# Performance work log

Measured on AMD Instinct MI355X. Metric: run time of the kernel, lower is better.

## Reference

```python
import jax, jax.numpy as jnp
import numpy as np

T, B, D = 2048, 16, 1024  # time, batch, hidden (input_size == output_size)
EPS = 1e-5


def setup_inputs() -> dict:
    key = jax.random.key(0)
    k1, k2 = jax.random.split(key, 2)
    inp = jax.random.normal(k1, (T, B, D), dtype=jnp.float32)
    # nn.Linear(D, 3D, bias=False); stored here as [in, out] so pre = x @ W
    W = jax.random.normal(k2, (D, 3 * D), dtype=jnp.float32) * (1.0 / np.sqrt(D))
    gamma = jnp.ones((3 * D,), dtype=jnp.float32)
    beta = jnp.zeros((3 * D,), dtype=jnp.float32)
    return {"input": inp, "W": W, "gamma": gamma, "beta": beta}


def _linrec(a, b, reverse=False):
    # h_t = a_t * h_{t-1} + b_t  (h_{-1} = 0), parallel prefix over time axis 0
    def comb(c1, c2):
        a1, b1 = c1
        a2, b2 = c2
        return a1 * a2, a2 * b1 + b2
    return jax.lax.associative_scan(comb, (a, b), axis=0, reverse=reverse)[1]


def reference(input, W, gamma, beta):
    d = input.shape[-1]
    pre = jnp.einsum('tbi,io->tbo', input, W)
    # LayerNorm over last dim (3*D)
    mu = pre.mean(-1, keepdims=True)
    var = pre.var(-1, keepdims=True)
    pre = (pre - mu) * jax.lax.rsqrt(var + EPS) * gamma + beta

    g = jax.nn.sigmoid(pre[..., :d])
    x = pre[..., d:2 * d]
    h_gate = jax.nn.sigmoid(pre[..., 2 * d:])

    half = d // 2
    gf, gb = g[..., :half], g[..., half:]
    xf, xb = x[..., :half], x[..., half:]

    h_f = _linrec(1.0 - gf, gf * xf)                 # forward-in-time scan
    h_b = _linrec(1.0 - gb, gb * xb, reverse=True)   # backward-in-time scan
    h = jnp.concatenate([h_f, h_b], axis=-1)         # [T,B,D]
    return (1.0 - h_gate) * h + input * h_gate
```

## Files before the change

### kernel.cpp

```cpp
#include <hip/hip_runtime.h>
#include <hip/hip_bf16.h>
#include <cstdint>

#define T_DIM 2048
#define B_DIM 16
#define D_DIM 1024
#define N3    (3*D_DIM)
#define M_ROWS (T_DIM*B_DIM)
#define HALF  (D_DIM/2)
#define SEG    64
#define SEGLEN (T_DIM/SEG)
#define NSEQ  (2*B_DIM*HALF)
#define NBLK  (N3/256)
#define GEMM_GRID ((M_ROWS/256)*NBLK)

typedef __attribute__((ext_vector_type(8))) short bf16x8;
typedef __attribute__((ext_vector_type(4))) float f32x4;

#define GLD_LDS16(g, l) __builtin_amdgcn_global_load_lds( \
    (const __attribute__((address_space(1))) void*)(g),   \
    (__attribute__((address_space(3))) void*)(l), 16, 0, 0)

__device__ __forceinline__ ushort f2bf(float x) {
    __hip_bfloat16 h = __float2bfloat16(x);
    return *reinterpret_cast<ushort*>(&h);
}

__device__ __forceinline__ float sigmoidf(float x) {
    return 1.0f / (1.0f + __expf(-x));
}

__device__ __forceinline__ float4 ln4(float4 v, float mu, float rs, float4 ga, float4 be) {
    float4 r;
    r.x = (v.x - mu) * rs * ga.x + be.x;
    r.y = (v.y - mu) * rs * ga.y + be.y;
    r.z = (v.z - mu) * rs * ga.z + be.z;
    r.w = (v.w - mu) * rs * ga.w + be.w;
    return r;
}

__device__ __forceinline__ float4 sig4(float4 v) {
    float4 r;
    r.x = sigmoidf(v.x); r.y = sigmoidf(v.y);
    r.z = sigmoidf(v.z); r.w = sigmoidf(v.w);
    return r;
}

__global__ __launch_bounds__(256) void cast_a(const float* __restrict__ in,
                                              ushort* __restrict__ out) {
    const size_t i = (size_t)blockIdx.x * 256 + threadIdx.x;
    const float4* p = (const float4*)in + i * 2;
    float4 a = p[0], b = p[1];
    float f[8] = {a.x, a.y, a.z, a.w, b.x, b.y, b.z, b.w};
    ushort r[8];
#pragma unroll
    for (int j = 0; j < 8; ++j) r[j] = f2bf(f[j]);
    *(uint4*)(out + i * 8) = *(const uint4*)r;
}

__global__ __launch_bounds__(256) void transpose_cast(const float* __restrict__ W,
                                                      ushort* __restrict__ WT) {
    __shared__ float tile[64][65];
    const int c0 = blockIdx.x * 64;
    const int r0 = blockIdx.y * 64;
    const int tr = threadIdx.x >> 6;
    const int tc = threadIdx.x & 63;
#pragma unroll
    for (int i = 0; i < 16; ++i) {
        const int r = tr + i * 4;
        tile[r][tc] = W[(size_t)(r0 + r) * N3 + c0 + tc];
    }
    __syncthreads();
#pragma unroll
    for (int i = 0; i < 16; ++i) {
        const int r = tr + i * 4;
        WT[(size_t)(c0 + r) * D_DIM + r0 + tc] = f2bf(tile[tc][r]);
    }
}

__global__ __launch_bounds__(512, 2) void gemm_bf16(const ushort* __restrict__ A,
                                                    const ushort* __restrict__ BT,
                                                    float* __restrict__ C,
                                                    float2* __restrict__ partial) {
    const int K = D_DIM;
    const int N = N3;
    __shared__ ushort As[2][256 * 64];
    __shared__ ushort Bs[2][256 * 64];
    const int tid  = threadIdx.x;
    const int wave = tid >> 6;
    const int lane = tid & 63;

    int bid = blockIdx.x;
    bid = (bid & 7) * (GEMM_GRID / 8) + (bid >> 3);
    const int m0    = (bid / NBLK) * 256;
    const int n_blk = bid % NBLK;
    const int n0    = n_blk * 256;

    const int wm = wave >> 2;
    const int wn = wave & 3;
    const int srow = lane >> 3;
    const int skc  = (((lane & 7) ^ srow) * 8);

    f32x4 acc[8][4] = {};
    bf16x8 af[8], bfr[4];

    const int q  = lane >> 4;
    const int lm = lane & 15;
    const int sw = lm & 7;

    auto stage = [&](int t, int p) {
#pragma unroll
        for (int it = 0; it < 4; ++it) {
            const int rb = it * 64 + wave * 8;
            GLD_LDS16(A  + (size_t)(m0 + rb + srow) * K + t * 64 + skc, &As[p][rb * 64]);
            GLD_LDS16(BT + (size_t)(n0 + rb + srow) * K + t * 64 + skc, &Bs[p][rb * 64]);
        }
    };
    auto read_frags = [&](int p, int ks) {
        const int ch = ((ks * 4 + q) ^ sw) * 8;
#pragma unroll
        for (int m = 0; m < 8; ++m)
            af[m] = *(const bf16x8*)&As[p][(wm * 128 + m * 16 + lm) * 64 + ch];
#pragma unroll
        for (int n = 0; n < 4; ++n)
            bfr[n] = *(const bf16x8*)&Bs[p][(wn * 64 + n * 16 + lm) * 64 + ch];
    };
    auto do_mfma = [&]() {
        __builtin_amdgcn_s_setprio(1);
#pragma unroll
        for (int m = 0; m < 8; ++m)
#pragma unroll
            for (int n = 0; n < 4; ++n)
                acc[m][n] = __builtin_amdgcn_mfma_f32_16x16x32_bf16(af[m], bfr[n], acc[m][n], 0, 0, 0);
        __builtin_amdgcn_s_setprio(0);
    };

    stage(0, 0);
    stage(1, 1);
    asm volatile("s_waitcnt vmcnt(8)" ::: "memory");
    __builtin_amdgcn_sched_barrier(0);
    __builtin_amdgcn_s_barrier();
    __builtin_amdgcn_sched_barrier(0);

#pragma unroll 2
    for (int t = 0; t < (K / 64) - 2; ++t) {
        const int p = t & 1;
        read_frags(p, 0);
        do_mfma();
        read_frags(p, 1);
        asm volatile("s_waitcnt lgkmcnt(0)" ::: "memory");
        __builtin_amdgcn_sched_barrier(0);
        __builtin_amdgcn_s_barrier();
        __builtin_amdgcn_sched_barrier(0);
        stage(t + 2, p);
        do_mfma();
        asm volatile("s_waitcnt vmcnt(8)" ::: "memory");
        __builtin_amdgcn_sched_barrier(0);
        __builtin_amdgcn_s_barrier();
        __builtin_amdgcn_sched_barrier(0);
    }
    read_frags(0, 0);
    do_mfma();
    read_frags(0, 1);
    do_mfma();
    asm volatile("s_waitcnt vmcnt(0)" ::: "memory");
    __builtin_amdgcn_sched_barrier(0);
    __builtin_amdgcn_s_barrier();
    __builtin_amdgcn_sched_barrier(0);
    read_frags(1, 0);
    do_mfma();
    read_frags(1, 1);
    do_mfma();

#pragma unroll
    for (int m = 0; m < 8; ++m) {
        const int row = m0 + wm * 128 + m * 16 + q * 4;
#pragma unroll
        for (int n = 0; n < 4; ++n) {
            const int col = n0 + wn * 64 + n * 16 + lm;
            float* cp = C + (size_t)row * N + col;
#pragma unroll
            for (int r = 0; r < 4; ++r)
                cp[(size_t)r * N] = acc[m][n][r];
        }
    }

    float* sS  = (float*)&As[0][0];
    float* sSS = sS + 1024;
#pragma unroll
    for (int m = 0; m < 8; ++m) {
#pragma unroll
        for (int r = 0; r < 4; ++r) {
            float s  = acc[m][0][r] + acc[m][1][r] + acc[m][2][r] + acc[m][3][r];
            float ss = acc[m][0][r] * acc[m][0][r] + acc[m][1][r] * acc[m][1][r]
                     + acc[m][2][r] * acc[m][2][r] + acc[m][3][r] * acc[m][3][r];
            s  += __shfl_xor(s, 1);  ss += __shfl_xor(ss, 1);
            s  += __shfl_xor(s, 2);  ss += __shfl_xor(ss, 2);
            s  += __shfl_xor(s, 4);  ss += __shfl_xor(ss, 4);
            s  += __shfl_xor(s, 8);  ss += __shfl_xor(ss, 8);
            if (lm == 0) {
                const int rl = wm * 128 + m * 16 + q * 4 + r;
                sS [wn * 256 + rl] = s;
                sSS[wn * 256 + rl] = ss;
            }
        }
    }
    __syncthreads();
    if (tid < 256) {
        const float S  = sS [tid] + sS [256 + tid] + sS [512 + tid] + sS [768 + tid];
        const float SS = sSS[tid] + sSS[256 + tid] + sSS[512 + tid] + sSS[768 + tid];
        partial[(size_t)n_blk * M_ROWS + m0 + tid] = make_float2(S, SS);
    }
}

__global__ __launch_bounds__(256) void finalize_stats(const float2* __restrict__ partial,
                                                      float2* __restrict__ stats) {
    const int row = blockIdx.x * 256 + threadIdx.x;
    float S = 0.f, SS = 0.f;
#pragma unroll
    for (int nb = 0; nb < NBLK; ++nb) {
        const float2 p = partial[(size_t)nb * M_ROWS + row];
        S += p.x; SS += p.y;
    }
    const float mu  = S * (1.0f / 3072.0f);
    const float var = SS * (1.0f / 3072.0f) - mu * mu;
    stats[row] = make_float2(mu, rsqrtf(var + 1e-5f));
}

__global__ __launch_bounds__(256) void scan_seg(const float* __restrict__ buf,
                                                const float2* __restrict__ stats,
                                                const float* __restrict__ gamma,
                                                const float* __restrict__ beta,
                                                float* __restrict__ segA,
                                                float* __restrict__ segB) {
    const int tid = threadIdx.x;
    const int s   = blockIdx.x;
    const int b   = blockIdx.y;
    const int dir = tid >> 7;
    const int cg4 = tid * 4;
    const float4 ga0 = *(const float4*)&gamma[cg4];
    const float4 be0 = *(const float4*)&beta [cg4];
    const float4 ga1 = *(const float4*)&gamma[cg4 + 1024];
    const float4 be1 = *(const float4*)&beta [cg4 + 1024];
    const size_t base = (size_t)b * N3 + cg4;
    float4 Aa = {1.f, 1.f, 1.f, 1.f};
    float4 Bb = {0.f, 0.f, 0.f, 0.f};

#define SEG_STEP(t)                                                         \
    {   const float2 st = stats[(t) * B_DIM + b];                           \
        const size_t idx = (size_t)(t) * (B_DIM * N3) + base;               \
        const float4 p0 = *(const float4*)&buf[idx];                        \
        const float4 p1 = *(const float4*)&buf[idx + 1024];                 \
        const float4 g  = sig4(ln4(p0, st.x, st.y, ga0, be0));              \
        const float4 xv = ln4(p1, st.x, st.y, ga1, be1);                    \
        Aa.x *= (1.f - g.x); Bb.x = (1.f - g.x) * Bb.x + g.x * xv.x;        \
        Aa.y *= (1.f - g.y); Bb.y = (1.f - g.y) * Bb.y + g.y * xv.y;        \
        Aa.z *= (1.f - g.z); Bb.z = (1.f - g.z) * Bb.z + g.z * xv.z;        \
        Aa.w *= (1.f - g.w); Bb.w = (1.f - g.w) * Bb.w + g.w * xv.w;        }

    if (dir == 0) {
#pragma unroll 4
        for (int i = 0; i < SEGLEN; ++i) SEG_STEP(s * SEGLEN + i);
    } else {
#pragma unroll 4
        for (int i = SEGLEN - 1; i >= 0; --i) SEG_STEP(s * SEGLEN + i);
    }
#undef SEG_STEP
    const int seq = (dir * 16 + b) * HALF + (cg4 - dir * 512);
    *(float4*)&segA[(size_t)s * NSEQ + seq] = Aa;
    *(float4*)&segB[(size_t)s * NSEQ + seq] = Bb;
}

__global__ __launch_bounds__(256) void scan_carry(const float* __restrict__ segA,
                                                  float* __restrict__ segB) {
    const int seq4 = (blockIdx.x * 256 + threadIdx.x) * 4;
    const int dir  = seq4 >> 13;
    float4 h = {0.f, 0.f, 0.f, 0.f};
#define CARRY_STEP(s)                                                       \
    {   const float4 Av = *(const float4*)&segA[(size_t)(s) * NSEQ + seq4]; \
        float4* bp = (float4*)&segB[(size_t)(s) * NSEQ + seq4];             \
        const float4 Bv = *bp;                                              \
        *bp = h;                                                            \
        h.x = Av.x * h.x + Bv.x; h.y = Av.y * h.y + Bv.y;                   \
        h.z = Av.z * h.z + Bv.z; h.w = Av.w * h.w + Bv.w;                   }
    if (dir == 0) {
        for (int s = 0; s < SEG; ++s) CARRY_STEP(s);
    } else {
        for (int s = SEG - 1; s >= 0; --s) CARRY_STEP(s);
    }
#undef CARRY_STEP
}

__global__ __launch_bounds__(256) void scan_apply(const float* __restrict__ buf,
                                                  const float2* __restrict__ stats,
                                                  const float* __restrict__ gamma,
                                                  const float* __restrict__ beta,
                                                  const float* __restrict__ segB,
                                                  const float* __restrict__ input,
                                                  float* __restrict__ out) {
    const int tid = threadIdx.x;
    const int s   = blockIdx.x;
    const int b   = blockIdx.y;
    const int dir = tid >> 7;
    const int cg4 = tid * 4;
    const float4 ga0 = *(const float4*)&gamma[cg4];
    const float4 be0 = *(const float4*)&beta [cg4];
    const float4 ga1 = *(const float4*)&gamma[cg4 + 1024];
    const float4 be1 = *(const float4*)&beta [cg4 + 1024];
    const float4 ga2 = *(const float4*)&gamma[cg4 + 2048];
    const float4 be2 = *(const float4*)&beta [cg4 + 2048];
    const int seq = (dir * 16 + b) * HALF + (cg4 - dir * 512);
    float4 h = *(const float4*)&segB[(size_t)s * NSEQ + seq];
    const size_t base3 = (size_t)b * N3 + cg4;
    const size_t base1 = (size_t)b * D_DIM + cg4;

#define APPLY_STEP(t)                                                       \
    {   const float2 st = stats[(t) * B_DIM + b];                           \
        const size_t i3 = (size_t)(t) * (B_DIM * N3) + base3;               \
        const size_t i1 = (size_t)(t) * (B_DIM * D_DIM) + base1;            \
        const float4 p0 = *(const float4*)&buf[i3];                         \
        const float4 p1 = *(const float4*)&buf[i3 + 1024];                  \
        const float4 p2 = *(const float4*)&buf[i3 + 2048];                  \
        const float4 iv = *(const float4*)&input[i1];                       \
        const float4 g  = sig4(ln4(p0, st.x, st.y, ga0, be0));              \
        const float4 xv = ln4(p1, st.x, st.y, ga1, be1);                    \
        const float4 hg = sig4(ln4(p2, st.x, st.y, ga2, be2));              \
        float4 o;                                                           \
        h.x = (1.f - g.x) * h.x + g.x * xv.x;                               \
        h.y = (1.f - g.y) * h.y + g.y * xv.y;                               \
        h.z = (1.f - g.z) * h.z + g.z * xv.z;                               \
        h.w = (1.f - g.w) * h.w + g.w * xv.w;                               \
        o.x = (1.f - hg.x) * h.x + iv.x * hg.x;                             \
        o.y = (1.f - hg.y) * h.y + iv.y * hg.y;                             \
        o.z = (1.f - hg.z) * h.z + iv.z * hg.z;                             \
        o.w = (1.f - hg.w) * h.w + iv.w * hg.w;                             \
        *(float4*)&out[i1] = o;                                             }

    if (dir == 0) {
#pragma unroll 4
        for (int i = 0; i < SEGLEN; ++i) APPLY_STEP(s * SEGLEN + i);
    } else {
#pragma unroll 4
        for (int i = SEGLEN - 1; i >= 0; --i) APPLY_STEP(s * SEGLEN + i);
    }
#undef APPLY_STEP
}

extern "C" void kernel_launch(void* const* d_in, const int* in_sizes, int n_in,
                              void* d_out, int out_size, void* d_ws, size_t ws_size,
                              hipStream_t stream) {
    const float* input = (const float*)d_in[0];
    const float* W     = (const float*)d_in[1];
    const float* gamma = (const float*)d_in[2];
    const float* beta  = (const float*)d_in[3];
    float* out = (float*)d_out;

    char* ws = (char*)d_ws;
    const size_t szA   = (size_t)M_ROWS * D_DIM * 2;
    const size_t szWT  = (size_t)N3 * D_DIM * 2;
    const size_t szBuf = (size_t)M_ROWS * N3 * 4;
    ushort* Abf  = (ushort*)ws;
    ushort* WT   = (ushort*)(ws + szA);
    float*  buf  = (float*)(ws + szA + szWT);
    float2* partial = (float2*)(ws + szA + szWT + szBuf);
    float2* stats   = (float2*)((char*)partial + (size_t)NBLK * M_ROWS * 8);
    float*  segA = (float*)ws;
    float*  segB = segA + (size_t)SEG * NSEQ;

    cast_a<<<(M_ROWS * D_DIM) / (256 * 8), 256, 0, stream>>>(input, Abf);
    transpose_cast<<<dim3(N3 / 64, D_DIM / 64), 256, 0, stream>>>(W, WT);
    gemm_bf16<<<GEMM_GRID, 512, 0, stream>>>(Abf, WT, buf, partial);
    finalize_stats<<<M_ROWS / 256, 256, 0, stream>>>(partial, stats);
    scan_seg<<<dim3(SEG, B_DIM), 256, 0, stream>>>(buf, stats, gamma, beta, segA, segB);
    scan_carry<<<NSEQ / 1024, 256, 0, stream>>>(segA, segB);
    scan_apply<<<dim3(SEG, B_DIM), 256, 0, stream>>>(buf, stats, gamma, beta, segB, input, out);
}
```

Baseline: 702.1 us.

## Load B fragments directly from pre-packed global layout, retune scan segments

W is repacked into MFMA fragment order so the GEMM loads B fragments straight from global memory into registers instead of staging them through LDS. A now uses a four-deep LDS ring. The scan is split into twice as many segments with deeper unrolling, and the carry pass runs one sequence per thread. Nontemporal loads and stores are used for the large intermediate and output buffers. Register B loads lose LDS sharing across waves and raise global traffic and register pressure.

```diff
diff --git a/kernel.cpp b/kernel.cpp
--- a/kernel.cpp
+++ b/kernel.cpp
@@ -8,7 +8,7 @@
 #define N3    (3*D_DIM)
 #define M_ROWS (T_DIM*B_DIM)
 #define HALF  (D_DIM/2)
-#define SEG    64
+#define SEG    128
 #define SEGLEN (T_DIM/SEG)
 #define NSEQ  (2*B_DIM*HALF)
 #define NBLK  (N3/256)
@@ -30,8 +30,8 @@
     return 1.0f / (1.0f + __expf(-x));
 }
 
-__device__ __forceinline__ float4 ln4(float4 v, float mu, float rs, float4 ga, float4 be) {
-    float4 r;
+__device__ __forceinline__ f32x4 ln4(f32x4 v, float mu, float rs, f32x4 ga, f32x4 be) {
+    f32x4 r;
     r.x = (v.x - mu) * rs * ga.x + be.x;
     r.y = (v.y - mu) * rs * ga.y + be.y;
     r.z = (v.z - mu) * rs * ga.z + be.z;
@@ -39,8 +39,8 @@
     return r;
 }
 
-__device__ __forceinline__ float4 sig4(float4 v) {
-    float4 r;
+__device__ __forceinline__ f32x4 sig4(f32x4 v) {
+    f32x4 r;
     r.x = sigmoidf(v.x); r.y = sigmoidf(v.y);
     r.z = sigmoidf(v.z); r.w = sigmoidf(v.w);
     return r;
@@ -49,8 +49,8 @@
 __global__ __launch_bounds__(256) void cast_a(const float* __restrict__ in,
                                               ushort* __restrict__ out) {
     const size_t i = (size_t)blockIdx.x * 256 + threadIdx.x;
-    const float4* p = (const float4*)in + i * 2;
-    float4 a = p[0], b = p[1];
+    const f32x4* p = (const f32x4*)in + i * 2;
+    f32x4 a = p[0], b = p[1];
     float f[8] = {a.x, a.y, a.z, a.w, b.x, b.y, b.z, b.w};
     ushort r[8];
 #pragma unroll
@@ -58,34 +58,29 @@
     *(uint4*)(out + i * 8) = *(const uint4*)r;
 }
 
-__global__ __launch_bounds__(256) void transpose_cast(const float* __restrict__ W,
-                                                      ushort* __restrict__ WT) {
-    __shared__ float tile[64][65];
-    const int c0 = blockIdx.x * 64;
-    const int r0 = blockIdx.y * 64;
-    const int tr = threadIdx.x >> 6;
-    const int tc = threadIdx.x & 63;
-#pragma unroll
-    for (int i = 0; i < 16; ++i) {
-        const int r = tr + i * 4;
-        tile[r][tc] = W[(size_t)(r0 + r) * N3 + c0 + tc];
-    }
-    __syncthreads();
-#pragma unroll
-    for (int i = 0; i < 16; ++i) {
-        const int r = tr + i * 4;
-        WT[(size_t)(c0 + r) * D_DIM + r0 + tc] = f2bf(tile[tc][r]);
-    }
+__global__ __launch_bounds__(256) void pack_b(const float* __restrict__ W,
+                                              ushort* __restrict__ PB) {
+    const int idx  = blockIdx.x * 256 + threadIdx.x;
+    const int lane = idx & 63;
+    const int gks  = idx >> 6;
+    const int ks   = gks & 31;
+    const int g    = gks >> 5;
+    const int lm = lane & 15, q = lane >> 4;
+    const int n  = g * 16 + lm;
+    const int k0 = ks * 32 + q * 8;
+    ushort r[8];
+#pragma unroll
+    for (int e = 0; e < 8; ++e) r[e] = f2bf(W[(size_t)(k0 + e) * N3 + n]);
+    *(uint4*)&PB[(size_t)idx * 8] = *(const uint4*)r;
 }
 
 __global__ __launch_bounds__(512, 2) void gemm_bf16(const ushort* __restrict__ A,
-                                                    const ushort* __restrict__ BT,
+                                                    const ushort* __restrict__ PB,
                                                     float* __restrict__ C,
                                                     float2* __restrict__ partial) {
     const int K = D_DIM;
     const int N = N3;
-    __shared__ ushort As[2][256 * 64];
-    __shared__ ushort Bs[2][256 * 64];
+    __shared__ ushort As[4][256 * 64];
     const int tid  = threadIdx.x;
     const int wave = tid >> 6;
     const int lane = tid & 63;
@@ -101,76 +96,76 @@
     const int srow = lane >> 3;
     const int skc  = (((lane & 7) ^ srow) * 8);
 
-    f32x4 acc[8][4] = {};
-    bf16x8 af[8], bfr[4];
-
     const int q  = lane >> 4;
     const int lm = lane & 15;
     const int sw = lm & 7;
-
-    auto stage = [&](int t, int p) {
+    const int ch0 = ((0 * 4 + q) ^ sw) * 8;
+    const int ch1 = ((1 * 4 + q) ^ sw) * 8;
+    const int gb  = (n0 >> 4) + wn * 4;
+
+    f32x4 acc[8][4] = {};
+    bf16x8 bA[8], bB[8];
+
+    auto stageA = [&](int t) {
+        const int ts = t > 15 ? 15 : t;
+        const int p  = t & 3;
 #pragma unroll
         for (int it = 0; it < 4; ++it) {
             const int rb = it * 64 + wave * 8;
-            GLD_LDS16(A  + (size_t)(m0 + rb + srow) * K + t * 64 + skc, &As[p][rb * 64]);
-            GLD_LDS16(BT + (size_t)(n0 + rb + srow) * K + t * 64 + skc, &Bs[p][rb * 64]);
+            GLD_LDS16(A + (size_t)(m0 + rb + srow) * K + ts * 64 + skc, &As[p][rb * 64]);
         }
     };
-    auto read_frags = [&](int p, int ks) {
-        const int ch = ((ks * 4 + q) ^ sw) * 8;
-#pragma unroll
-        for (int m = 0; m < 8; ++m)
-            af[m] = *(const bf16x8*)&As[p][(wm * 128 + m * 16 + lm) * 64 + ch];
+    auto loadB = [&](int t, bf16x8* dst) {
+        const int tb = t > 15 ? 15 : t;
 #pragma unroll
         for (int n = 0; n < 4; ++n)
-            bfr[n] = *(const bf16x8*)&Bs[p][(wn * 64 + n * 16 + lm) * 64 + ch];
+#pragma unroll
+            for (int ks = 0; ks < 2; ++ks)
+                dst[n * 2 + ks] = *(const bf16x8*)&PB[((((size_t)gb + n) * 32 + 2 * tb + ks) * 64 + lane) * 8];
     };
-    auto do_mfma = [&]() {
-        __builtin_amdgcn_s_setprio(1);
-#pragma unroll
-        for (int m = 0; m < 8; ++m)
-#pragma unroll
-            for (int n = 0; n < 4; ++n)
-                acc[m][n] = __builtin_amdgcn_mfma_f32_16x16x32_bf16(af[m], bfr[n], acc[m][n], 0, 0, 0);
-        __builtin_amdgcn_s_setprio(0);
+    auto TILE = [&](int t, bf16x8* bc, bf16x8* bn) {
+        stageA(t + 2);
+        loadB(t + 1, bn);
+        const ushort* Ab = &As[t & 3][0];
+#pragma unroll
+        for (int mq = 0; mq < 4; ++mq) {
+            const int r0 = (wm * 128 + (2 * mq) * 16 + lm) * 64;
+            const int r1 = (wm * 128 + (2 * mq + 1) * 16 + lm) * 64;
+            bf16x8 a00 = *(const bf16x8*)&Ab[r0 + ch0];
+            bf16x8 a10 = *(const bf16x8*)&Ab[r1 + ch0];
+            bf16x8 a01 = *(const bf16x8*)&Ab[r0 + ch1];
+            bf16x8 a11 = *(const bf16x8*)&Ab[r1 + ch1];
+            __builtin_amdgcn_s_setprio(1);
+#pragma unroll
+            for (int n = 0; n < 4; ++n) {
+                acc[2 * mq][n]     = __builtin_amdgcn_mfma_f32_16x16x32_bf16(a00, bc[n * 2],     acc[2 * mq][n],     0, 0, 0);
+                acc[2 * mq + 1][n] = __builtin_amdgcn_mfma_f32_16x16x32_bf16(a10, bc[n * 2],     acc[2 * mq + 1][n], 0, 0, 0);
+                acc[2 * mq][n]     = __builtin_amdgcn_mfma_f32_16x16x32_bf16(a01, bc[n * 2 + 1], acc[2 * mq][n],     0, 0, 0);
+                acc[2 * mq + 1][n] = __builtin_amdgcn_mfma_f32_16x16x32_bf16(a11, bc[n * 2 + 1], acc[2 * mq + 1][n], 0, 0, 0);
+            }
+            __builtin_amdgcn_s_setprio(0);
+        }
+        asm volatile("s_waitcnt vmcnt(12)" ::: "memory");
+        __builtin_amdgcn_sched_barrier(0);
+        __builtin_amdgcn_s_barrier();
+        __builtin_amdgcn_sched_barrier(0);
     };
 
-    stage(0, 0);
-    stage(1, 1);
-    asm volatile("s_waitcnt vmcnt(8)" ::: "memory");
+    stageA(0);
+    stageA(1);
+    loadB(0, bA);
+    asm volatile("s_waitcnt vmcnt(12)" ::: "memory");
     __builtin_amdgcn_sched_barrier(0);
     __builtin_amdgcn_s_barrier();
     __builtin_amdgcn_sched_barrier(0);
 
-#pragma unroll 2
-    for (int t = 0; t < (K / 64) - 2; ++t) {
-        const int p = t & 1;
-        read_frags(p, 0);
-        do_mfma();
-        read_frags(p, 1);
-        asm volatile("s_waitcnt lgkmcnt(0)" ::: "memory");
-        __builtin_amdgcn_sched_barrier(0);
-        __builtin_amdgcn_s_barrier();
-        __builtin_amdgcn_sched_barrier(0);
-        stage(t + 2, p);
-        do_mfma();
-        asm volatile("s_waitcnt vmcnt(8)" ::: "memory");
-        __builtin_amdgcn_sched_barrier(0);
-        __builtin_amdgcn_s_barrier();
-        __builtin_amdgcn_sched_barrier(0);
-    }
-    read_frags(0, 0);
-    do_mfma();
-    read_frags(0, 1);
-    do_mfma();
-    asm volatile("s_waitcnt vmcnt(0)" ::: "memory");
-    __builtin_amdgcn_sched_barrier(0);
-    __builtin_amdgcn_s_barrier();
-    __builtin_amdgcn_sched_barrier(0);
-    read_frags(1, 0);
-    do_mfma();
-    read_frags(1, 1);
-    do_mfma();
+#pragma unroll 1
+    for (int tt = 0; tt < 8; ++tt) {
+        TILE(2 * tt,     bA, bB);
+        TILE(2 * tt + 1, bB, bA);
+    }
+
+    __syncthreads();
 
 #pragma unroll
     for (int m = 0; m < 8; ++m) {
@@ -181,7 +176,7 @@
             float* cp = C + (size_t)row * N + col;
 #pragma unroll
             for (int r = 0; r < 4; ++r)
-                cp[(size_t)r * N] = acc[m][n][r];
+                __builtin_nontemporal_store(acc[m][n][r], cp + (size_t)r * N);
         }
     }
 
@@ -238,57 +233,59 @@
     const int b   = blockIdx.y;
     const int dir = tid >> 7;
     const int cg4 = tid * 4;
-    const float4 ga0 = *(const float4*)&gamma[cg4];
-    const float4 be0 = *(const float4*)&beta [cg4];
-    const float4 ga1 = *(const float4*)&gamma[cg4 + 1024];
-    const float4 be1 = *(const float4*)&beta [cg4 + 1024];
+    const f32x4 ga0 = *(const f32x4*)&gamma[cg4];
+    const f32x4 be0 = *(const f32x4*)&beta [cg4];
+    const f32x4 ga1 = *(const f32x4*)&gamma[cg4 + 1024];
+    const f32x4 be1 = *(const f32x4*)&beta [cg4 + 1024];
     const size_t base = (size_t)b * N3 + cg4;
-    float4 Aa = {1.f, 1.f, 1.f, 1.f};
-    float4 Bb = {0.f, 0.f, 0.f, 0.f};
+    f32x4 Aa = {1.f, 1.f, 1.f, 1.f};
+    f32x4 Bb = {0.f, 0.f, 0.f, 0.f};
 
 #define SEG_STEP(t)                                                         \
     {   const float2 st = stats[(t) * B_DIM + b];                           \
         const size_t idx = (size_t)(t) * (B_DIM * N3) + base;               \
-        const float4 p0 = *(const float4*)&buf[idx];                        \
-        const float4 p1 = *(const float4*)&buf[idx + 1024];                 \
-        const float4 g  = sig4(ln4(p0, st.x, st.y, ga0, be0));              \
-        const float4 xv = ln4(p1, st.x, st.y, ga1, be1);                    \
+        const f32x4 p0 = __builtin_nontemporal_load((const f32x4*)&buf[idx]);        \
+        const f32x4 p1 = __builtin_nontemporal_load((const f32x4*)&buf[idx + 1024]); \
+        const f32x4 g  = sig4(ln4(p0, st.x, st.y, ga0, be0));               \
+        const f32x4 xv = ln4(p1, st.x, st.y, ga1, be1);                     \
         Aa.x *= (1.f - g.x); Bb.x = (1.f - g.x) * Bb.x + g.x * xv.x;        \
         Aa.y *= (1.f - g.y); Bb.y = (1.f - g.y) * Bb.y + g.y * xv.y;        \
         Aa.z *= (1.f - g.z); Bb.z = (1.f - g.z) * Bb.z + g.z * xv.z;        \
         Aa.w *= (1.f - g.w); Bb.w = (1.f - g.w) * Bb.w + g.w * xv.w;        }
 
     if (dir == 0) {
-#pragma unroll 4
+#pragma unroll 8
         for (int i = 0; i < SEGLEN; ++i) SEG_STEP(s * SEGLEN + i);
     } else {
-#pragma unroll 4
+#pragma unroll 8
         for (int i = SEGLEN - 1; i >= 0; --i) SEG_STEP(s * SEGLEN + i);
     }
 #undef SEG_STEP
     const int seq = (dir * 16 + b) * HALF + (cg4 - dir * 512);
-    *(float4*)&segA[(size_t)s * NSEQ + seq] = Aa;
-    *(float4*)&segB[(size_t)s * NSEQ + seq] = Bb;
+    *(f32x4*)&segA[(size_t)s * NSEQ + seq] = Aa;
+    *(f32x4*)&segB[(size_t)s * NSEQ + seq] = Bb;
 }
 
 __global__ __launch_bounds__(256) void scan_carry(const float* __restrict__ segA,
                                                   float* __restrict__ segB) {
-    const int seq4 = (blockIdx.x * 256 + threadIdx.x) * 4;
-    const int dir  = seq4 >> 13;
-    float4 h = {0.f, 0.f, 0.f, 0.f};
-#define CARRY_STEP(s)                                                       \
-    {   const float4 Av = *(const float4*)&segA[(size_t)(s) * NSEQ + seq4]; \
-        float4* bp = (float4*)&segB[(size_t)(s) * NSEQ + seq4];             \
-        const float4 Bv = *bp;                                              \
-        *bp = h;                                                            \
-        h.x = Av.x * h.x + Bv.x; h.y = Av.y * h.y + Bv.y;                   \
-        h.z = Av.z * h.z + Bv.z; h.w = Av.w * h.w + Bv.w;                   }
+    const int seq = blockIdx.x * 256 + threadIdx.x;
+    const int dir = seq >> 13;
+    float h = 0.f;
     if (dir == 0) {
-        for (int s = 0; s < SEG; ++s) CARRY_STEP(s);
+        for (int s = 0; s < SEG; ++s) {
+            const float Av = segA[(size_t)s * NSEQ + seq];
+            const float Bv = segB[(size_t)s * NSEQ + seq];
+            segB[(size_t)s * NSEQ + seq] = h;
+            h = Av * h + Bv;
+        }
     } else {
-        for (int s = SEG - 1; s >= 0; --s) CARRY_STEP(s);
-    }
-#undef CARRY_STEP
+        for (int s = SEG - 1; s >= 0; --s) {
+            const float Av = segA[(size_t)s * NSEQ + seq];
+            const float Bv = segB[(size_t)s * NSEQ + seq];
+            segB[(size_t)s * NSEQ + seq] = h;
+            h = Av * h + Bv;
+        }
+    }
 }
 
 __global__ __launch_bounds__(256) void scan_apply(const float* __restrict__ buf,
@@ -303,14 +300,14 @@
     const int b   = blockIdx.y;
     const int dir = tid >> 7;
     const int cg4 = tid * 4;
-    const float4 ga0 = *(const float4*)&gamma[cg4];
-    const float4 be0 = *(const float4*)&beta [cg4];
-    const float4 ga1 = *(const float4*)&gamma[cg4 + 1024];
-    const float4 be1 = *(const float4*)&beta [cg4 + 1024];
-    const float4 ga2 = *(const float4*)&gamma[cg4 + 2048];
-    const float4 be2 = *(const float4*)&beta [cg4 + 2048];
+    const f32x4 ga0 = *(const f32x4*)&gamma[cg4];
+    const f32x4 be0 = *(const f32x4*)&beta [cg4];
+    const f32x4 ga1 = *(const f32x4*)&gamma[cg4 + 1024];
+    const f32x4 be1 = *(const f32x4*)&beta [cg4 + 1024];
+    const f32x4 ga2 = *(const f32x4*)&gamma[cg4 + 2048];
+    const f32x4 be2 = *(const f32x4*)&beta [cg4 + 2048];
     const int seq = (dir * 16 + b) * HALF + (cg4 - dir * 512);
-    float4 h = *(const float4*)&segB[(size_t)s * NSEQ + seq];
+    f32x4 h = *(const f32x4*)&segB[(size_t)s * NSEQ + seq];
     const size_t base3 = (size_t)b * N3 + cg4;
     const size_t base1 = (size_t)b * D_DIM + cg4;
 
@@ -318,14 +315,14 @@
     {   const float2 st = stats[(t) * B_DIM + b];                           \
         const size_t i3 = (size_t)(t) * (B_DIM * N3) + base3;               \
         const size_t i1 = (size_t)(t) * (B_DIM * D_DIM) + base1;            \
-        const float4 p0 = *(const float4*)&buf[i3];                         \
-        const float4 p1 = *(const float4*)&buf[i3 + 1024];                  \
-        const float4 p2 = *(const float4*)&buf[i3 + 2048];                  \
-        const float4 iv = *(const float4*)&input[i1];                       \
-        const float4 g  = sig4(ln4(p0, st.x, st.y, ga0, be0));              \
-        const float4 xv = ln4(p1, st.x, st.y, ga1, be1);                    \
-        const float4 hg = sig4(ln4(p2, st.x, st.y, ga2, be2));              \
-        float4 o;                                                           \
+        const f32x4 p0 = __builtin_nontemporal_load((const f32x4*)&buf[i3]);         \
+        const f32x4 p1 = __builtin_nontemporal_load((const f32x4*)&buf[i3 + 1024]);  \
+        const f32x4 p2 = __builtin_nontemporal_load((const f32x4*)&buf[i3 + 2048]);  \
+        const f32x4 iv = *(const f32x4*)&input[i1];                         \
+        const f32x4 g  = sig4(ln4(p0, st.x, st.y, ga0, be0));               \
+        const f32x4 xv = ln4(p1, st.x, st.y, ga1, be1);                     \
+        const f32x4 hg = sig4(ln4(p2, st.x, st.y, ga2, be2));               \
+        f32x4 o;                                                            \
         h.x = (1.f - g.x) * h.x + g.x * xv.x;                               \
         h.y = (1.f - g.y) * h.y + g.y * xv.y;                               \
         h.z = (1.f - g.z) * h.z + g.z * xv.z;                               \
@@ -334,13 +331,13 @@
         o.y = (1.f - hg.y) * h.y + iv.y * hg.y;                             \
         o.z = (1.f - hg.z) * h.z + iv.z * hg.z;                             \
         o.w = (1.f - hg.w) * h.w + iv.w * hg.w;                             \
-        *(float4*)&out[i1] = o;                                             }
+        __builtin_nontemporal_store(o, (f32x4*)&out[i1]);                   }
 
     if (dir == 0) {
-#pragma unroll 4
+#pragma unroll 8
         for (int i = 0; i < SEGLEN; ++i) APPLY_STEP(s * SEGLEN + i);
     } else {
-#pragma unroll 4
+#pragma unroll 8
         for (int i = SEGLEN - 1; i >= 0; --i) APPLY_STEP(s * SEGLEN + i);
     }
 #undef APPLY_STEP
@@ -357,21 +354,21 @@
 
     char* ws = (char*)d_ws;
     const size_t szA   = (size_t)M_ROWS * D_DIM * 2;
-    const size_t szWT  = (size_t)N3 * D_DIM * 2;
+    const size_t szPB  = (size_t)N3 * D_DIM * 2;
     const size_t szBuf = (size_t)M_ROWS * N3 * 4;
     ushort* Abf  = (ushort*)ws;
-    ushort* WT   = (ushort*)(ws + szA);
-    float*  buf  = (float*)(ws + szA + szWT);
-    float2* partial = (float2*)(ws + szA + szWT + szBuf);
+    ushort* PB   = (ushort*)(ws + szA);
+    float*  buf  = (float*)(ws + szA + szPB);
+    float2* partial = (float2*)(ws + szA + szPB + szBuf);
     float2* stats   = (float2*)((char*)partial + (size_t)NBLK * M_ROWS * 8);
     float*  segA = (float*)ws;
     float*  segB = segA + (size_t)SEG * NSEQ;
 
     cast_a<<<(M_ROWS * D_DIM) / (256 * 8), 256, 0, stream>>>(input, Abf);
-    transpose_cast<<<dim3(N3 / 64, D_DIM / 64), 256, 0, stream>>>(W, WT);
-    gemm_bf16<<<GEMM_GRID, 512, 0, stream>>>(Abf, WT, buf, partial);
+    pack_b<<<(N3 / 16) * 32 * 64 / 256, 256, 0, stream>>>(W, PB);
+    gemm_bf16<<<GEMM_GRID, 512, 0, stream>>>(Abf, PB, buf, partial);
     finalize_stats<<<M_ROWS / 256, 256, 0, stream>>>(partial, stats);
     scan_seg<<<dim3(SEG, B_DIM), 256, 0, stream>>>(buf, stats, gamma, beta, segA, segB);
-    scan_carry<<<NSEQ / 1024, 256, 0, stream>>>(segA, segB);
+    scan_carry<<<NSEQ / 256, 256, 0, stream>>>(segA, segB);
     scan_apply<<<dim3(SEG, B_DIM), 256, 0, stream>>>(buf, stats, gamma, beta, segB, input, out);
 }
```

Measured after the change: 662.6 us. 1.06x faster.
